# Optimization experiments

Hardware: AMD Instinct MI355X
Metric: run time of the kernel (lower is better)

## Reference

```python
import jax, jax.numpy as jnp
import numpy as np

B, C, H, W = 2, 256, 64, 64
NH = 4          # num_heads -> ch = C // NH = 64
G = 32          # GroupNorm groups (normalization(channels))
EPS = 1e-5


def setup_inputs() -> dict:
    key = jax.random.key(0)
    ks = jax.random.split(key, 7)
    s = 1.0 / np.sqrt(C).astype(np.float32)
    return {
        "x": jax.random.normal(ks[0], (B, C, H, W), jnp.float32),
        "gn_scale": 1.0 + 0.02 * jax.random.normal(ks[1], (C,), jnp.float32),
        "gn_bias": 0.02 * jax.random.normal(ks[2], (C,), jnp.float32),
        "w_qkv": s * jax.random.normal(ks[3], (3 * C, C), jnp.float32),
        "b_qkv": jnp.zeros((3 * C,), jnp.float32),
        # NOTE: original zero-inits proj_out; we use random weights so the
        # attention path contributes to the output (meaningful baseline).
        "w_proj": s * jax.random.normal(ks[4], (C, C), jnp.float32),
        "b_proj": jnp.zeros((C,), jnp.float32),
    }


def reference(x, gn_scale, gn_bias, w_qkv, b_qkv, w_proj, b_proj):
    b, c = x.shape[0], x.shape[1]
    spatial = x.shape[2:]
    t = int(np.prod(spatial))
    xf = x.reshape(b, c, t)                      # [B, C, T]

    # GroupNorm(32) over (channels-in-group, T)
    xg = xf.reshape(b, G, c // G, t)
    mu = xg.mean(axis=(2, 3), keepdims=True)
    var = xg.var(axis=(2, 3), keepdims=True)
    xn = ((xg - mu) * jax.lax.rsqrt(var + EPS)).reshape(b, c, t)
    xn = xn * gn_scale[None, :, None] + gn_bias[None, :, None]

    # 1x1 conv -> qkv: [B, 3C, T]
    qkv = jnp.einsum('oc,bct->bot', w_qkv, xn) + b_qkv[None, :, None]

    # QKVAttentionLegacy: reshape (B*H, 3*ch, T) then split
    ch = c // NH
    qkv_h = qkv.reshape(b * NH, 3 * ch, t)
    q, k, v = jnp.split(qkv_h, 3, axis=1)        # each [B*H, ch, T]
    scale = 1.0 / np.sqrt(np.sqrt(ch)).astype(np.float32)
    w = jnp.einsum('bct,bcs->bts', q * scale, k * scale)   # [B*H, T, T]
    w = jax.nn.softmax(w.astype(jnp.float32), axis=-1).astype(qkv.dtype)
    a = jnp.einsum('bts,bcs->bct', w, v).reshape(b, c, t)  # [B, C, T]

    # proj 1x1 conv + residual
    h = jnp.einsum('oc,bct->bot', w_proj, a) + b_proj[None, :, None]
    return (xf + h).reshape(b, c, *spatial)
```

## Files before the change

kernel.cpp:

```cpp
#include <hip/hip_runtime.h>
#include <math.h>

#define T 4096
#define C 256
#define BATCH 2
#define NH 4
#define G 32
#define CPG 8
#define EPS 1e-5f
#define LOG2E 1.4426950408889634f
#define QSCALE (0.125f * LOG2E)
#define KSPLIT 4
#define KRANGE (T / KSPLIT)
#define BH (BATCH * NH)

typedef __attribute__((ext_vector_type(8))) short bfv8;
typedef __attribute__((ext_vector_type(4))) short bfv4;
typedef __attribute__((ext_vector_type(4))) float f32x4;

static __device__ __forceinline__ short f2bf(float f) {
    union { float f; unsigned u; } v; v.f = f;
    return (short)((v.u + 0x7FFFu + ((v.u >> 16) & 1u)) >> 16);
}
static __device__ __forceinline__ short f2bf_fast(float f) {
    union { float f; unsigned u; } v; v.f = f;
    return (short)((v.u + 0x8000u) >> 16);
}
static __device__ __forceinline__ float bf2f(short s) {
    union { float f; unsigned u; } v; v.u = ((unsigned)(unsigned short)s) << 16;
    return v.f;
}

#if __has_builtin(__builtin_amdgcn_exp2f)
#define EXP2(x) __builtin_amdgcn_exp2f(x)
#else
#define EXP2(x) exp2f(x)
#endif

#define AS1 __attribute__((address_space(1)))
#define AS3 __attribute__((address_space(3)))
static __device__ __forceinline__ void gll16(const void* g, void* l) {
    __builtin_amdgcn_global_load_lds((const AS1 void*)g, (AS3 void*)l, 16, 0, 0);
}

__global__ __launch_bounds__(256) void prep_w(const float* __restrict__ wq,
                                              const float* __restrict__ wp,
                                              short* __restrict__ wqb,
                                              short* __restrict__ wpb) {
    int i = blockIdx.x * 256 + threadIdx.x;
    const int NQ = 768 * 256 / 4;
    float4 v; short* dst;
    if (i < NQ) { v = ((const float4*)wq)[i]; dst = wqb + i * 4; }
    else        { int j = i - NQ; v = ((const float4*)wp)[j]; dst = wpb + j * 4; }
    bfv4 o = { f2bf(v.x), f2bf(v.y), f2bf(v.z), f2bf(v.w) };
    *(bfv4*)dst = o;
}

__global__ __launch_bounds__(256) void gn_stats(const float* __restrict__ x,
                                                float* __restrict__ gnp) {
    const int blk = blockIdx.x;
    const int ts  = blockIdx.y;
    const int b = blk / G, g = blk % G;
    const float* xp = x + ((size_t)b * C + g * CPG) * T + ts * 1024;

    const int tid = threadIdx.x;
    float s = 0.f, ss = 0.f;
    #pragma unroll
    for (int u = 0; u < CPG; u++) {
        float4 v = ((const float4*)(xp + (size_t)u * T))[tid];
        s  += v.x + v.y + v.z + v.w;
        ss += v.x*v.x + v.y*v.y + v.z*v.z + v.w*v.w;
    }
    __shared__ float rs[256], rss[256];
    rs[tid] = s; rss[tid] = ss;
    __syncthreads();
    for (int off = 128; off > 0; off >>= 1) {
        if (tid < off) { rs[tid] += rs[tid+off]; rss[tid] += rss[tid+off]; }
        __syncthreads();
    }
    if (tid == 0) {
        gnp[(blk * 4 + ts) * 2 + 0] = rs[0];
        gnp[(blk * 4 + ts) * 2 + 1] = rss[0];
    }
}

__global__ __launch_bounds__(256) void gn_norm(const float* __restrict__ x,
                                               const float* __restrict__ scale,
                                               const float* __restrict__ bias,
                                               const float* __restrict__ gnp,
                                               short* __restrict__ xnT) {
    const int blk = blockIdx.x;
    const int ts  = blockIdx.y;
    const int b = blk / G, g = blk % G;
    const int c0 = g * CPG;
    const float* xp = x + ((size_t)b * C + c0) * T;

    float s = 0.f, ss = 0.f;
    #pragma unroll
    for (int i = 0; i < 4; i++) {
        s  += gnp[(blk * 4 + i) * 2 + 0];
        ss += gnp[(blk * 4 + i) * 2 + 1];
    }
    const float inv_n = 1.0f / (CPG * T);
    const float mu  = s * inv_n;
    const float var = ss * inv_n - mu * mu;
    const float rstd = rsqrtf(var + EPS);

    float sc[CPG], bi[CPG];
    #pragma unroll
    for (int u = 0; u < CPG; u++) {
        sc[u] = scale[c0+u] * rstd;
        bi[u] = bias[c0+u] - mu * sc[u];
    }

    const int t = ts * 1024 + threadIdx.x * 4;
    float vv[CPG][4];
    #pragma unroll
    for (int u = 0; u < CPG; u++) {
        float4 v = *(const float4*)&xp[(size_t)u * T + t];
        vv[u][0] = v.x * sc[u] + bi[u];
        vv[u][1] = v.y * sc[u] + bi[u];
        vv[u][2] = v.z * sc[u] + bi[u];
        vv[u][3] = v.w * sc[u] + bi[u];
    }
    #pragma unroll
    for (int j = 0; j < 4; j++) {
        bfv8 w = { f2bf(vv[0][j]), f2bf(vv[1][j]), f2bf(vv[2][j]), f2bf(vv[3][j]),
                   f2bf(vv[4][j]), f2bf(vv[5][j]), f2bf(vv[6][j]), f2bf(vv[7][j]) };
        *(bfv8*)&xnT[((size_t)b * T + t + j) * C + c0] = w;
    }
}

__global__ __launch_bounds__(256) void gemm_qkv(
    const short* __restrict__ wq,
    const float* __restrict__ bq,
    const short* __restrict__ xnT,
    short* __restrict__ qb, short* __restrict__ kb, short* __restrict__ vb)
{
    const int b  = blockIdx.z;
    const int t0 = blockIdx.x * 64;
    const int ot = blockIdx.y;
    const int h = ot / 3, part = ot % 3;
    const int o0 = ot * 64;

    __shared__ short sm[4096];
    short* Ab = sm;
    short* Bb = sm + 2048;

    const int tid = threadIdx.x, lane = tid & 63, wave = tid >> 6;
    const int col = lane & 15, quad = lane >> 4;
    const short* xb = xnT + (size_t)b * T * C;

    f32x4 acc[4];
    #pragma unroll
    for (int g = 0; g < 4; g++) { acc[g][0]=0.f; acc[g][1]=0.f; acc[g][2]=0.f; acc[g][3]=0.f; }

    for (int k0 = 0; k0 < C; k0 += 32) {
        __syncthreads();
        gll16(wq + (size_t)(o0 + 16*wave + col) * C + k0 + quad*8, Ab + wave*512);
        gll16(xb + (size_t)(t0 + 16*wave + col) * C + k0 + quad*8, Bb + wave*512);
        __syncthreads();
        bfv8 af = *(const bfv8*)(Ab + wave*512 + lane*8);
        #pragma unroll
        for (int g = 0; g < 4; g++) {
            bfv8 bf = *(const bfv8*)(Bb + g*512 + lane*8);
            acc[g] = __builtin_amdgcn_mfma_f32_16x16x32_bf16(af, bf, acc[g], 0, 0, 0);
        }
    }

    const int olocal = 16*wave + quad*4;
    float bias_r[4];
    #pragma unroll
    for (int r = 0; r < 4; r++) bias_r[r] = bq[o0 + olocal + r];
    const size_t hd = (size_t)(b * NH + h);

    if (part < 2) {
        short* dst = (part == 0 ? qb : kb) + hd * T * 64;
        const float sc = (part == 0) ? QSCALE : 1.0f;
        #pragma unroll
        for (int g = 0; g < 4; g++) {
            int t = t0 + 16*g + col;
            bfv4 w = { f2bf((acc[g][0] + bias_r[0]) * sc),
                       f2bf((acc[g][1] + bias_r[1]) * sc),
                       f2bf((acc[g][2] + bias_r[2]) * sc),
                       f2bf((acc[g][3] + bias_r[3]) * sc) };
            *(bfv4*)&dst[(size_t)t * 64 + olocal] = w;
        }
    } else {
        short* dst = vb + hd * 64 * T;
        #pragma unroll
        for (int g = 0; g < 4; g++)
            #pragma unroll
            for (int r = 0; r < 4; r++)
                dst[(size_t)(olocal + r) * T + t0 + 16*g + col] =
                    f2bf(acc[g][r] + bias_r[r]);
    }
}

__global__ __launch_bounds__(256) void attn_kernel(
    const short* __restrict__ qb,
    const short* __restrict__ kb,
    const short* __restrict__ vb,
    short* __restrict__ opart,
    float* __restrict__ lp)
{
    __shared__ short smem[20992];
    const int bh = blockIdx.y;
    const int ks = blockIdx.z;
    const int t0 = blockIdx.x * 64;
    const int k0base = ks * KRANGE;
    const short* kbh = kb + (size_t)bh * T * 64;
    const short* vbh = vb + (size_t)bh * 64 * T;

    const int tid  = threadIdx.x;
    const int lane = tid & 63;
    const int wave = tid >> 6;
    const int col  = lane & 15;
    const int quad = lane >> 4;

    const short* qrow = qb + (size_t)bh * T * 64 + (size_t)(t0 + wave*16 + col) * 64;
    bfv8 qf0 = *(const bfv8*)(qrow + quad*8);
    bfv8 qf1 = *(const bfv8*)(qrow + 32 + quad*8);

    f32x4 oacc[4];
    #pragma unroll
    for (int g = 0; g < 4; g++) { oacc[g][0]=0.f; oacc[g][1]=0.f; oacc[g][2]=0.f; oacc[g][3]=0.f; }
    float lpart[4] = {0.f, 0.f, 0.f, 0.f};

    short* pW = smem + 16384 + wave * 1152;

    #define STAGE_KV(buf, s0)                                                  \
        {                                                                      \
            short* base = smem + (buf) * 8192;                                 \
            _Pragma("unroll")                                                  \
            for (int u = 0; u < 2; u++) {                                      \
                gll16(kbh + (size_t)((s0) + 16*wave + col) * 64 + (quad + 4*u)*8, \
                      base + (wave + 4*u) * 512);                              \
                gll16(vbh + (size_t)(16*wave + col) * T + (s0) + (quad + 4*u)*8, \
                      base + 4096 + (wave + 4*u) * 512);                       \
            }                                                                  \
        }

    STAGE_KV(0, k0base)

    for (int it = 0; it < KRANGE/64; it++) {
        __syncthreads();
        if (it + 1 < KRANGE/64) STAGE_KV((it+1) & 1, k0base + (it+1)*64)

        const short* kvb = smem + (it & 1) * 8192;

        f32x4 s[4];
        #pragma unroll
        for (int g = 0; g < 4; g++) {
            bfv8 kf0 = *(const bfv8*)(kvb + g*512 + lane*8);
            bfv8 kf1 = *(const bfv8*)(kvb + (4+g)*512 + lane*8);
            f32x4 a0 = {0.f, 0.f, 0.f, 0.f};
            a0 = __builtin_amdgcn_mfma_f32_16x16x32_bf16(qf0, kf0, a0, 0, 0, 0);
            a0 = __builtin_amdgcn_mfma_f32_16x16x32_bf16(qf1, kf1, a0, 0, 0, 0);
            s[g] = a0;
        }

        #pragma unroll
        for (int g = 0; g < 4; g++)
            #pragma unroll
            for (int r = 0; r < 4; r++) {
                float p = EXP2(s[g][r]);
                s[g][r] = p;
                lpart[r] += p;
            }

        #pragma unroll
        for (int g = 0; g < 4; g++)
            #pragma unroll
            for (int r = 0; r < 4; r++)
                pW[(quad*4 + r)*72 + 16*g + col] = f2bf_fast(s[g][r]);

        bfv8 pf0 = *(const bfv8*)&pW[col*72 + quad*8];
        bfv8 pf1 = *(const bfv8*)&pW[col*72 + 32 + quad*8];

        #pragma unroll
        for (int g = 0; g < 4; g++) {
            bfv8 vf0 = *(const bfv8*)(kvb + 4096 + g*512 + lane*8);
            bfv8 vf1 = *(const bfv8*)(kvb + 4096 + (4+g)*512 + lane*8);
            oacc[g] = __builtin_amdgcn_mfma_f32_16x16x32_bf16(pf0, vf0, oacc[g], 0, 0, 0);
            oacc[g] = __builtin_amdgcn_mfma_f32_16x16x32_bf16(pf1, vf1, oacc[g], 0, 0, 0);
        }
    }

    #pragma unroll
    for (int off = 1; off < 16; off <<= 1)
        #pragma unroll
        for (int r = 0; r < 4; r++)
            lpart[r] += __shfl_xor(lpart[r], off);

    const size_t rowbase = (size_t)(ks*BH + bh) * T + t0 + wave*16;
    short* opb = opart + rowbase * 64;
    #pragma unroll
    for (int g = 0; g < 4; g++)
        #pragma unroll
        for (int r = 0; r < 4; r++)
            opb[(size_t)(quad*4 + r) * 64 + 16*g + col] = f2bf(oacc[g][r]);
    if (col == 0) {
        #pragma unroll
        for (int r = 0; r < 4; r++)
            lp[rowbase + quad*4 + r] = lpart[r];
    }
}

__global__ __launch_bounds__(256) void combine_kernel(
    const short* __restrict__ opart, const float* __restrict__ lp,
    short* __restrict__ aT)
{
    const int bh = blockIdx.y;
    const int b = bh >> 2, h = bh & 3;
    const int q = blockIdx.x * 64 + (threadIdx.x >> 2);
    const int cg = (threadIdx.x & 3) * 16;

    float lsum = 0.f;
    #pragma unroll
    for (int ks = 0; ks < KSPLIT; ks++)
        lsum += lp[(size_t)(ks*BH + bh) * T + q];
    const float rl = 1.0f / lsum;

    float acc[16] = {};
    #pragma unroll
    for (int ks = 0; ks < KSPLIT; ks++) {
        const short* p = opart + ((size_t)(ks*BH + bh) * T + q) * 64 + cg;
        bfv8 a0 = *(const bfv8*)p, a1 = *(const bfv8*)(p + 8);
        #pragma unroll
        for (int u = 0; u < 8; u++) { acc[u] += bf2f(a0[u]); acc[u+8] += bf2f(a1[u]); }
    }
    short ov[16];
    #pragma unroll
    for (int u = 0; u < 16; u++) ov[u] = f2bf(acc[u] * rl);
    short* ap = aT + ((size_t)b * T + q) * C + h*64 + cg;
    *(bfv8*)ap       = *(bfv8*)&ov[0];
    *(bfv8*)(ap + 8) = *(bfv8*)&ov[8];
}

__global__ __launch_bounds__(256) void gemm_proj(
    const short* __restrict__ wp,
    const float* __restrict__ bp,
    const short* __restrict__ aT,
    const float* __restrict__ x,
    float* __restrict__ out)
{
    const int b  = blockIdx.z;
    const int t0 = blockIdx.x * 64;
    const int o0 = blockIdx.y * 64;

    __shared__ short sm[4096];
    short* Ab = sm;
    short* Bb = sm + 2048;

    const int tid = threadIdx.x, lane = tid & 63, wave = tid >> 6;
    const int col = lane & 15, quad = lane >> 4;
    const short* ab = aT + (size_t)b * T * C;

    f32x4 acc[4];
    #pragma unroll
    for (int g = 0; g < 4; g++) { acc[g][0]=0.f; acc[g][1]=0.f; acc[g][2]=0.f; acc[g][3]=0.f; }

    for (int k0 = 0; k0 < C; k0 += 32) {
        __syncthreads();
        gll16(wp + (size_t)(o0 + 16*wave + col) * C + k0 + quad*8, Ab + wave*512);
        gll16(ab + (size_t)(t0 + 16*wave + col) * C + k0 + quad*8, Bb + wave*512);
        __syncthreads();
        bfv8 af = *(const bfv8*)(Ab + wave*512 + lane*8);
        #pragma unroll
        for (int g = 0; g < 4; g++) {
            bfv8 bf = *(const bfv8*)(Bb + g*512 + lane*8);
            acc[g] = __builtin_amdgcn_mfma_f32_16x16x32_bf16(af, bf, acc[g], 0, 0, 0);
        }
    }

    const int olocal = 16*wave + quad*4;
    #pragma unroll
    for (int r = 0; r < 4; r++) {
        const int o = o0 + olocal + r;
        const float bias = bp[o];
        const size_t rowoff = ((size_t)b * C + o) * T;
        #pragma unroll
        for (int g = 0; g < 4; g++) {
            const size_t idx = rowoff + t0 + 16*g + col;
            out[idx] = acc[g][r] + bias + x[idx];
        }
    }
}

extern "C" void kernel_launch(void* const* d_in, const int* in_sizes, int n_in,
                              void* d_out, int out_size, void* d_ws, size_t ws_size,
                              hipStream_t stream) {
    (void)in_sizes; (void)n_in; (void)out_size; (void)ws_size;
    const float* x        = (const float*)d_in[0];
    const float* gn_scale = (const float*)d_in[1];
    const float* gn_bias  = (const float*)d_in[2];
    const float* w_qkv    = (const float*)d_in[3];
    const float* b_qkv    = (const float*)d_in[4];
    const float* w_proj   = (const float*)d_in[5];
    const float* b_proj   = (const float*)d_in[6];
    float* out = (float*)d_out;

    short* ws    = (short*)d_ws;
    short* qb    = ws;
    short* kb    = qb  + (size_t)BH * T * 64;
    short* vb    = kb  + (size_t)BH * T * 64;
    short* aT    = vb  + (size_t)BH * T * 64;
    short* xnT   = aT  + (size_t)BATCH * T * C;
    short* wqb   = xnT + (size_t)BATCH * T * C;
    short* wpb   = wqb + 768 * 256;
    short* opart = wpb + 256 * 256;
    float* lp    = (float*)(opart + (size_t)KSPLIT * BH * T * 64);
    float* gnp   = lp + (size_t)KSPLIT * BH * T;

    prep_w<<<dim3(256), 256, 0, stream>>>(w_qkv, w_proj, wqb, wpb);
    gn_stats<<<dim3(BATCH * G, 4), 256, 0, stream>>>(x, gnp);
    gn_norm<<<dim3(BATCH * G, 4), 256, 0, stream>>>(x, gn_scale, gn_bias, gnp, xnT);
    gemm_qkv<<<dim3(T/64, 12, BATCH), 256, 0, stream>>>(wqb, b_qkv, xnT, qb, kb, vb);
    attn_kernel<<<dim3(T/64, BH, KSPLIT), 256, 0, stream>>>(qb, kb, vb, opart, lp);
    combine_kernel<<<dim3(T/64, BH), 256, 0, stream>>>(opart, lp, aT);
    gemm_proj<<<dim3(T/64, 4, BATCH), 256, 0, stream>>>(wpb, b_proj, aT, x, out);
}
```

Measured before the change: 177.3 us.

## Fuse split-K attention combine into projection GEMM and deepen K tile

Removes the separate combine kernel: the projection GEMM now reads the split-K partial attention outputs and row sums directly, normalizes them while staging its B tile in shared memory, and skips the intermediate aT buffer. Both GEMMs also process 64 K-elements per barrier pair instead of 32, halving synchronization. The trade-off is that each of the 4 output-channel blocks in gemm_proj re-reads and re-reduces the partials (4x redundant combine reads), and the B loads become synchronous register loads instead of direct-to-LDS copies.

```diff
diff --git a/kernel.cpp b/kernel.cpp
--- a/kernel.cpp
+++ b/kernel.cpp
@@ -143,9 +143,9 @@
     const int h = ot / 3, part = ot % 3;
     const int o0 = ot * 64;
 
-    __shared__ short sm[4096];
+    __shared__ short sm[8192];
     short* Ab = sm;
-    short* Bb = sm + 2048;
+    short* Bb = sm + 4096;
 
     const int tid = threadIdx.x, lane = tid & 63, wave = tid >> 6;
     const int col = lane & 15, quad = lane >> 4;
@@ -155,16 +155,24 @@
     #pragma unroll
     for (int g = 0; g < 4; g++) { acc[g][0]=0.f; acc[g][1]=0.f; acc[g][2]=0.f; acc[g][3]=0.f; }
 
-    for (int k0 = 0; k0 < C; k0 += 32) {
-        __syncthreads();
-        gll16(wq + (size_t)(o0 + 16*wave + col) * C + k0 + quad*8, Ab + wave*512);
-        gll16(xb + (size_t)(t0 + 16*wave + col) * C + k0 + quad*8, Bb + wave*512);
-        __syncthreads();
-        bfv8 af = *(const bfv8*)(Ab + wave*512 + lane*8);
-        #pragma unroll
-        for (int g = 0; g < 4; g++) {
-            bfv8 bf = *(const bfv8*)(Bb + g*512 + lane*8);
-            acc[g] = __builtin_amdgcn_mfma_f32_16x16x32_bf16(af, bf, acc[g], 0, 0, 0);
+    for (int k0 = 0; k0 < C; k0 += 64) {
+        __syncthreads();
+        #pragma unroll
+        for (int hh = 0; hh < 2; hh++) {
+            gll16(wq + (size_t)(o0 + 16*wave + col) * C + k0 + hh*32 + quad*8,
+                  Ab + (hh*4 + wave) * 512);
+            gll16(xb + (size_t)(t0 + 16*wave + col) * C + k0 + hh*32 + quad*8,
+                  Bb + (hh*4 + wave) * 512);
+        }
+        __syncthreads();
+        #pragma unroll
+        for (int hh = 0; hh < 2; hh++) {
+            bfv8 af = *(const bfv8*)(Ab + (hh*4 + wave) * 512 + lane*8);
+            #pragma unroll
+            for (int g = 0; g < 4; g++) {
+                bfv8 bf = *(const bfv8*)(Bb + (hh*4 + g) * 512 + lane*8);
+                acc[g] = __builtin_amdgcn_mfma_f32_16x16x32_bf16(af, bf, acc[g], 0, 0, 0);
+            }
         }
     }
 
@@ -307,41 +315,11 @@
     }
 }
 
-__global__ __launch_bounds__(256) void combine_kernel(
-    const short* __restrict__ opart, const float* __restrict__ lp,
-    short* __restrict__ aT)
-{
-    const int bh = blockIdx.y;
-    const int b = bh >> 2, h = bh & 3;
-    const int q = blockIdx.x * 64 + (threadIdx.x >> 2);
-    const int cg = (threadIdx.x & 3) * 16;
-
-    float lsum = 0.f;
-    #pragma unroll
-    for (int ks = 0; ks < KSPLIT; ks++)
-        lsum += lp[(size_t)(ks*BH + bh) * T + q];
-    const float rl = 1.0f / lsum;
-
-    float acc[16] = {};
-    #pragma unroll
-    for (int ks = 0; ks < KSPLIT; ks++) {
-        const short* p = opart + ((size_t)(ks*BH + bh) * T + q) * 64 + cg;
-        bfv8 a0 = *(const bfv8*)p, a1 = *(const bfv8*)(p + 8);
-        #pragma unroll
-        for (int u = 0; u < 8; u++) { acc[u] += bf2f(a0[u]); acc[u+8] += bf2f(a1[u]); }
-    }
-    short ov[16];
-    #pragma unroll
-    for (int u = 0; u < 16; u++) ov[u] = f2bf(acc[u] * rl);
-    short* ap = aT + ((size_t)b * T + q) * C + h*64 + cg;
-    *(bfv8*)ap       = *(bfv8*)&ov[0];
-    *(bfv8*)(ap + 8) = *(bfv8*)&ov[8];
-}
-
 __global__ __launch_bounds__(256) void gemm_proj(
     const short* __restrict__ wp,
     const float* __restrict__ bp,
-    const short* __restrict__ aT,
+    const short* __restrict__ opart,
+    const float* __restrict__ lp,
     const float* __restrict__ x,
     float* __restrict__ out)
 {
@@ -349,28 +327,59 @@
     const int t0 = blockIdx.x * 64;
     const int o0 = blockIdx.y * 64;
 
-    __shared__ short sm[4096];
+    __shared__ short sm[8192];
     short* Ab = sm;
-    short* Bb = sm + 2048;
+    short* Bb = sm + 4096;
 
     const int tid = threadIdx.x, lane = tid & 63, wave = tid >> 6;
     const int col = lane & 15, quad = lane >> 4;
-    const short* ab = aT + (size_t)b * T * C;
+
+    const int trow = t0 + 16*wave + col;
+    float rl4[NH];
+    #pragma unroll
+    for (int hh = 0; hh < NH; hh++) {
+        float ls = 0.f;
+        #pragma unroll
+        for (int ks = 0; ks < KSPLIT; ks++)
+            ls += lp[((size_t)(ks*BH) + b*NH + hh) * T + trow];
+        rl4[hh] = 1.0f / ls;
+    }
 
     f32x4 acc[4];
     #pragma unroll
     for (int g = 0; g < 4; g++) { acc[g][0]=0.f; acc[g][1]=0.f; acc[g][2]=0.f; acc[g][3]=0.f; }
 
-    for (int k0 = 0; k0 < C; k0 += 32) {
-        __syncthreads();
-        gll16(wp + (size_t)(o0 + 16*wave + col) * C + k0 + quad*8, Ab + wave*512);
-        gll16(ab + (size_t)(t0 + 16*wave + col) * C + k0 + quad*8, Bb + wave*512);
-        __syncthreads();
-        bfv8 af = *(const bfv8*)(Ab + wave*512 + lane*8);
-        #pragma unroll
-        for (int g = 0; g < 4; g++) {
-            bfv8 bf = *(const bfv8*)(Bb + g*512 + lane*8);
-            acc[g] = __builtin_amdgcn_mfma_f32_16x16x32_bf16(af, bf, acc[g], 0, 0, 0);
+    for (int k0 = 0; k0 < C; k0 += 64) {
+        __syncthreads();
+        #pragma unroll
+        for (int hh = 0; hh < 2; hh++) {
+            gll16(wp + (size_t)(o0 + 16*wave + col) * C + k0 + hh*32 + quad*8,
+                  Ab + (hh*4 + wave) * 512);
+            const int chg = k0 + hh*32 + quad*8;
+            const int hd = chg >> 6, chin = chg & 63;
+            const short* ob = opart + (((size_t)(b*NH + hd)) * T + trow) * 64 + chin;
+            float a8[8] = {0.f,0.f,0.f,0.f,0.f,0.f,0.f,0.f};
+            #pragma unroll
+            for (int ks = 0; ks < KSPLIT; ks++) {
+                bfv8 v = *(const bfv8*)(ob + (size_t)ks * BH * T * 64);
+                #pragma unroll
+                for (int u = 0; u < 8; u++) a8[u] += bf2f(v[u]);
+            }
+            const float rl = rl4[hd];
+            bfv8 pk;
+            #pragma unroll
+            for (int u = 0; u < 8; u++) pk[u] = f2bf(a8[u] * rl);
+            *(bfv8*)(Bb + (hh*4 + wave) * 512 + lane*8) = pk;
+        }
+        __syncthreads();
+        #pragma unroll
+        for (int hh = 0; hh < 2; hh++) {
+            bfv8 af = *(const bfv8*)(Ab + (hh*4 + wave) * 512 + lane*8);
+            #pragma unroll
+            for (int g = 0; g < 4; g++) {
+                bfv8 bf = *(const bfv8*)(Bb + (hh*4 + g) * 512 + lane*8);
+                acc[g] = __builtin_amdgcn_mfma_f32_16x16x32_bf16(af, bf, acc[g], 0, 0, 0);
+            }
         }
     }
 
@@ -405,8 +414,7 @@
     short* qb    = ws;
     short* kb    = qb  + (size_t)BH * T * 64;
     short* vb    = kb  + (size_t)BH * T * 64;
-    short* aT    = vb  + (size_t)BH * T * 64;
-    short* xnT   = aT  + (size_t)BATCH * T * C;
+    short* xnT   = vb  + (size_t)BH * T * 64;
     short* wqb   = xnT + (size_t)BATCH * T * C;
     short* wpb   = wqb + 768 * 256;
     short* opart = wpb + 256 * 256;
@@ -418,6 +426,5 @@
     gn_norm<<<dim3(BATCH * G, 4), 256, 0, stream>>>(x, gn_scale, gn_bias, gnp, xnT);
     gemm_qkv<<<dim3(T/64, 12, BATCH), 256, 0, stream>>>(wqb, b_qkv, xnT, qb, kb, vb);
     attn_kernel<<<dim3(T/64, BH, KSPLIT), 256, 0, stream>>>(qb, kb, vb, opart, lp);
-    combine_kernel<<<dim3(T/64, BH), 256, 0, stream>>>(opart, lp, aT);
-    gemm_proj<<<dim3(T/64, 4, BATCH), 256, 0, stream>>>(wpb, b_proj, aT, x, out);
-}
+    gemm_proj<<<dim3(T/64, 4, BATCH), 256, 0, stream>>>(wpb, b_proj, opart, lp, x, out);
+}
```

Result: no change. 176.1 us (-0.7%).
